# Kernel tuning notes

Measured on AMD Instinct MI355X. Metric: run time of the kernel, lower is better.

## Reference

```python
import jax, jax.numpy as jnp
import numpy as np

B, N = 128, 512            # graphs per batch, nodes (seq len) per graph
NODE_VOCAB, APP_VOCAB = 30000, 5000
D, R, K = 128, 512, 3      # embed_size, rec_embed dim, Chebyshev order
EPS = 1e-12


def setup_inputs() -> dict:
    key = jax.random.key(0)
    ks = jax.random.split(key, 8)
    return {
        # all tokens nonzero -> every position is a valid node (item > 0 filter passes)
        "input_seq": jax.random.randint(ks[0], (B, N), 1, NODE_VOCAB),
        "recd_token": jax.random.randint(ks[1], (B, N), 1, APP_VOCAB),
        "embed_table": jax.random.normal(ks[2], (NODE_VOCAB, D), jnp.float32) * 0.02,
        "rec_embed_table": jax.random.normal(ks[3], (APP_VOCAB, R), jnp.float32) * 0.02,
        "cheb_w1": jax.random.normal(ks[4], (K, D, D), jnp.float32) / np.sqrt(D),
        "cheb_b1": jnp.zeros((D,), jnp.float32),
        "cheb_w2": jax.random.normal(ks[5], (K, D, D), jnp.float32) / np.sqrt(D),
        "cheb_b2": jnp.zeros((D,), jnp.float32),
    }


def _prop_matrix(app_emb):
    """Per-sample scaled Laplacian L_hat = -D^{-1/2} A D^{-1/2}.

    app_emb: [B,N,R] (detached upstream, matching recd.detach() in the source).
    Adjacency: cosine-sim matrix, entries below the mean of the nonzero strict
    upper triangle zeroed. ChebConv receives edge_index only -> binary weights,
    self-loops removed, default lambda_max=2 -> L_hat = -A_norm.
    """
    app_feat = app_emb / jnp.maximum(
        jnp.linalg.norm(app_emb, axis=-1, keepdims=True), EPS)      # F.normalize dim=1
    A = jnp.einsum('bnr,bmr->bnm', app_feat, app_feat)              # [B,N,N]
    upper = jnp.triu(A, 1)
    cnt = jnp.sum(upper != 0, axis=(1, 2)).astype(A.dtype)
    mean = jnp.sum(upper, axis=(1, 2)) / jnp.maximum(cnt, 1.0)      # [B]
    A = jnp.where(A < mean[:, None, None], 0.0, A)
    adj = (A != 0).astype(A.dtype) * (1.0 - jnp.eye(N, dtype=A.dtype))  # binary, no self-loops
    deg = adj.sum(-1)                                               # [B,N]
    dinv = jnp.where(deg > 0, jax.lax.rsqrt(jnp.maximum(deg, EPS)), 0.0)
    return -(dinv[:, :, None] * adj * dinv[:, None, :])             # [B,N,N]


def _cheb(x, S, w, b):
    # Chebyshev recurrence T0=x, T1=Sx, T2=2S T1 - T0
    tx0 = x
    tx1 = jnp.einsum('bnm,bmd->bnd', S, tx0)
    tx2 = 2.0 * jnp.einsum('bnm,bmd->bnd', S, tx1) - tx0
    return (jnp.einsum('bnd,de->bne', tx0, w[0])
            + jnp.einsum('bnd,de->bne', tx1, w[1])
            + jnp.einsum('bnd,de->bne', tx2, w[2]) + b)


def reference(input_seq, recd_token, embed_table, rec_embed_table,
              cheb_w1, cheb_b1, cheb_w2, cheb_b2):
    app_emb = rec_embed_table[recd_token]                           # [B,N,R]
    # adjacency built from detached embeddings (recd.detach() in source)
    S = jax.lax.stop_gradient(_prop_matrix(jax.lax.stop_gradient(app_emb)))
    x = embed_table[input_seq]                                      # [B,N,D]
    x = jax.nn.relu(_cheb(x, S, cheb_w1, cheb_b1))
    x = jax.nn.relu(_cheb(x, S, cheb_w2, cheb_b2))
    out = jnp.concatenate([x, app_emb], axis=-1)                    # [B,N,D+R]
    return out.reshape(B * N, D + R)                                # Batch'ed node features
```

## Files before the change

### kernel.cpp

```cpp
#include <hip/hip_runtime.h>
#include <hip/hip_bf16.h>

typedef __attribute__((ext_vector_type(8))) unsigned short ushort8;
typedef __attribute__((ext_vector_type(4))) unsigned short bf16x4;
typedef __attribute__((ext_vector_type(8))) short short8;
typedef __attribute__((ext_vector_type(4))) float f32x4;
typedef __attribute__((ext_vector_type(2))) unsigned long long u64x2;

#define DEV __device__ __forceinline__

DEV unsigned short f2bf(float f) {
    unsigned u = __builtin_bit_cast(unsigned, f);
    return (unsigned short)((u + 0x7fffu + ((u >> 16) & 1u)) >> 16);
}
DEV float bf2f(unsigned short h) {
    unsigned u = ((unsigned)h) << 16;
    return __builtin_bit_cast(float, u);
}
DEV float wred(float v) {
#pragma unroll
    for (int m = 32; m > 0; m >>= 1) v += __shfl_xor(v, m, 64);
    return v;
}

constexpr int N_ = 512, D_ = 128, R_ = 512;
constexpr long NN2 = (long)N_ * N_;

DEV void gll16(const void* g, void* l) {
    __builtin_amdgcn_global_load_lds(
        (const __attribute__((address_space(1))) unsigned*)g,
        (__attribute__((address_space(3))) unsigned*)l, 16, 0, 0);
}


__global__ __launch_bounds__(256) void k_front(const int* __restrict__ recd,
                                               const float* __restrict__ rtab,
                                               const int* __restrict__ seq,
                                               const float* __restrict__ etab,
                                               const float* __restrict__ w1,
                                               const float* __restrict__ w2,
                                               float* __restrict__ out,
                                               unsigned short* __restrict__ feat,
                                               unsigned short* __restrict__ x,
                                               unsigned short* __restrict__ wT) {
    int bid = blockIdx.x, tid = threadIdx.x;
    if (bid < 16384) {
        int lane = tid & 63, w = tid >> 6;
        long r = (long)bid * 4 + w;
        int tok = recd[r];
        const float* src = rtab + (long)tok * R_;
        int j = lane * 8;
        float4 v0 = *(const float4*)(src + j);
        float4 v1 = *(const float4*)(src + j + 4);
        float ssq = v0.x*v0.x + v0.y*v0.y + v0.z*v0.z + v0.w*v0.w
                  + v1.x*v1.x + v1.y*v1.y + v1.z*v1.z + v1.w*v1.w;
        ssq = wred(ssq);
        float sc = 1.0f / fmaxf(sqrtf(ssq), 1e-12f);
        float* o = out + r * 640 + 128 + j;
        *(float4*)o = v0;
        *(float4*)(o + 4) = v1;
        ushort8 u;
        u[0]=f2bf(v0.x*sc); u[1]=f2bf(v0.y*sc); u[2]=f2bf(v0.z*sc); u[3]=f2bf(v0.w*sc);
        u[4]=f2bf(v1.x*sc); u[5]=f2bf(v1.y*sc); u[6]=f2bf(v1.z*sc); u[7]=f2bf(v1.w*sc);
        *(ushort8*)(feat + r * R_ + j) = u;
    } else if (bid < 20480) {
        long e8 = ((long)(bid - 16384) * 256 + tid) * 8;
        long r = e8 >> 7;
        int d0 = (int)(e8 & 127);
        int tok = seq[r];
        const float* src = etab + (long)tok * D_ + d0;
        float4 v0 = *(const float4*)src, v1 = *(const float4*)(src + 4);
        ushort8 u;
        u[0]=f2bf(v0.x); u[1]=f2bf(v0.y); u[2]=f2bf(v0.z); u[3]=f2bf(v0.w);
        u[4]=f2bf(v1.x); u[5]=f2bf(v1.y); u[6]=f2bf(v1.z); u[7]=f2bf(v1.w);
        *(ushort8*)(x + e8) = u;
    } else {
        int o = (bid - 20480) * 256 + tid;
        int l = o / 49152;
        int rr = o - l * 49152;
        int mat = rr >> 14;
        int e2 = rr & 16383;
        int e = e2 >> 7, d = e2 & 127;
        const float* w = l ? w2 : w1;
        float v;
        if (mat == 0)      v = w[d * 128 + e] - w[32768 + d * 128 + e];
        else if (mat == 1) v = w[16384 + d * 128 + e];
        else               v = 2.0f * w[32768 + d * 128 + e];
        wT[o] = f2bf(v);
    }
}


DEV void stage_rowmajor(const unsigned short* base, long ld, int k0,
                        unsigned short* dst, int tid) {
#pragma unroll
    for (int i = 0; i < 4; ++i) {
        int u = i * 256 + tid;
        int r = u >> 3, c = (u & 7) * 8;
        gll16(base + (long)r * ld + k0 + c,
              dst + i * 2048 + (tid & 448) * 8);
    }
}

DEV void gemm_bt_core(const unsigned short* Abase, long ldA,
                      const unsigned short* Bbase, long ldB, int K,
                      unsigned short* As, unsigned short* Bs,
                      f32x4 acc[4][4], bool dual) {
    int tid = threadIdx.x, lane = tid & 63, wave = tid >> 6;
    int wm = wave >> 1, wn = wave & 1;
    int fr = lane & 15, ko = (lane >> 4) * 8;
    const unsigned short* Bsrc = dual ? Bs : As;
    for (int k0 = 0; k0 < K; k0 += 64) {
        __syncthreads();
        stage_rowmajor(Abase, ldA, k0, As, tid);
        if (dual) stage_rowmajor(Bbase, ldB, k0, Bs, tid);
        __syncthreads();
#pragma unroll
        for (int ks = 0; ks < 2; ++ks) {
            short8 a[4], b[4];
#pragma unroll
            for (int m = 0; m < 4; ++m)
                a[m] = *(const short8*)(As + (wm * 64 + m * 16 + fr) * 64 + ks * 32 + ko);
#pragma unroll
            for (int n = 0; n < 4; ++n)
                b[n] = *(const short8*)(Bsrc + (wn * 64 + n * 16 + fr) * 64 + ks * 32 + ko);
#pragma unroll
            for (int m = 0; m < 4; ++m)
#pragma unroll
                for (int n = 0; n < 4; ++n)
                    acc[m][n] = __builtin_amdgcn_mfma_f32_16x16x32_bf16(
                        a[m], b[n], acc[m][n], 0, 0, 0);
        }
    }
}


__global__ __launch_bounds__(256) void k_adj(const unsigned short* __restrict__ feat,
                                             unsigned short* __restrict__ Abf,
                                             float* __restrict__ psum,
                                             float* __restrict__ pcnt) {
    __shared__ unsigned short As[128 * 64], Bs[128 * 64];
    __shared__ float sred[4], cred[4];
    int g = blockIdx.x;
    int r = g & 7, q = g >> 3;
    int q10 = q / 10;
    int b = r + (q10 << 3);
    int t = q - q10 * 10;
    int tm = (t < 4) ? 0 : (t < 7) ? 1 : (t < 9) ? 2 : 3;
    int tn = t - (tm * (9 - tm)) / 2 + tm;
    bool diag = (tm == tn);
    const unsigned short* fb = feat + (long)b * NN2;
    f32x4 acc[4][4] = {};
    gemm_bt_core(fb + (long)tm * 128 * R_, R_, fb + (long)tn * 128 * R_, R_, R_,
                 As, Bs, acc, !diag);
    int tid = threadIdx.x, lane = tid & 63, wave = tid >> 6;
    int wm = wave >> 1, wn = wave & 1;
    float s = 0.f, c = 0.f;
    unsigned short* Ab = Abf + (long)b * NN2;
#pragma unroll
    for (int m = 0; m < 4; ++m)
#pragma unroll
        for (int n = 0; n < 4; ++n) {
            f32x4 v = acc[m][n];
            int gj = tn * 128 + wn * 64 + n * 16 + (lane & 15);
            int gi0 = tm * 128 + wm * 64 + m * 16 + (lane >> 4) * 4;
            bf16x4 tw;
#pragma unroll
            for (int qq = 0; qq < 4; ++qq) {
                int gi = gi0 + qq;
                unsigned short bv = f2bf(v[qq]);
                Ab[(long)gi * N_ + gj] = bv;
                tw[qq] = bv;
                if (gj > gi) {
                    s += v[qq];
                    c += (v[qq] != 0.0f) ? 1.0f : 0.0f;
                }
            }
            if (!diag)
                *(bf16x4*)(Ab + (long)gj * N_ + gi0) = tw;
        }
    s = wred(s);
    c = wred(c);
    if (lane == 0) { sred[wave] = s; cred[wave] = c; }
    __syncthreads();
    if (tid == 0) {
        psum[b * 16 + t] = sred[0] + sred[1] + sred[2] + sred[3];
        pcnt[b * 16 + t] = cred[0] + cred[1] + cred[2] + cred[3];
    }
}

__global__ __launch_bounds__(256) void k_degtrs(unsigned short* __restrict__ Abf,
                                                const float* __restrict__ psum,
                                                const float* __restrict__ pcnt,
                                                const unsigned short* __restrict__ xin,
                                                float* __restrict__ dinv,
                                                unsigned short* __restrict__ pT) {
    __shared__ unsigned char mb[4][64];
    __shared__ float sdinv[64];
    __shared__ unsigned short t[64 * 128];
    int bid = blockIdx.x;
    int b = bid >> 3, tn = bid & 7;
    int tid = threadIdx.x, lane = tid & 63, w = tid >> 6;
    float s = 0.f, c = 0.f;
#pragma unroll
    for (int k = 0; k < 10; ++k) { s += psum[b * 16 + k]; c += pcnt[b * 16 + k]; }
    float m = s / fmaxf(c, 1.0f);
#pragma unroll 1
    for (int i = 0; i < 16; ++i) {
        int rl = w * 16 + i;
        long r = (long)b * 512 + tn * 64 + rl;
        int ig = tn * 64 + rl;
        ushort8 v = *(const ushort8*)(Abf + r * 512 + lane * 8);
        unsigned byt = 0;
        int cnt = 0;
#pragma unroll
        for (int k = 0; k < 8; ++k) {
            float f = bf2f(v[k]);
            int j = lane * 8 + k;
            bool keep = (f >= m) && (f != 0.0f) && (j != ig);
            byt |= (keep ? 1u : 0u) << k;
            cnt += keep ? 1 : 0;
        }
        mb[w][lane] = (unsigned char)byt;
        float fc = wred((float)cnt);
        if (lane < 8) {
            unsigned long long mword = *(const unsigned long long*)&mb[w][lane * 8];
            *(unsigned long long*)((unsigned char*)Abf + r * 1024 + lane * 8) = mword;
        }
        if (lane == 8) {
            float dv = (fc > 0.f) ? rsqrtf(fc) : 0.f;
            dinv[r] = dv;
            sdinv[rl] = dv;
        }
    }
    __syncthreads();
    const unsigned short* ib = xin + ((long)b * 512 + tn * 64) * 128;
    unsigned short* ob = pT + (long)b * 65536 + tn * 64;
#pragma unroll
    for (int i = 0; i < 4; ++i) {
        int u = i * 256 + tid;
        int n = u >> 4, g = u & 15;
        float sc = sdinv[n];
        ushort8 v = *(const ushort8*)(ib + n * 128 + g * 8);
        ushort8 sv;
#pragma unroll
        for (int tt = 0; tt < 8; ++tt) sv[tt] = f2bf(bf2f(v[tt]) * sc);
        int gs = g ^ ((n >> 3) & 7);
        *(ushort8*)(t + n * 128 + gs * 8) = sv;
    }
    __syncthreads();
#pragma unroll
    for (int i = 0; i < 4; ++i) {
        int u = i * 256 + tid;
        int d = u >> 3, n8 = (u & 7) * 8;
        ushort8 v;
#pragma unroll
        for (int tt = 0; tt < 8; ++tt) {
            int n = n8 + tt;
            int g = (d >> 3) ^ ((n >> 3) & 7);
            v[tt] = t[n * 128 + g * 8 + (d & 7)];
        }
        *(ushort8*)(ob + (long)d * 512 + n8) = v;
    }
}

__global__ __launch_bounds__(256) void k_sxm(const unsigned short* __restrict__ Abf,
                                             const float* __restrict__ dinv,
                                             const unsigned short* __restrict__ pT,
                                             unsigned short* __restrict__ outN,
                                             unsigned short* __restrict__ outT) {
    __shared__ __align__(16) unsigned short Bs[128 * 64];
    __shared__ __align__(8) unsigned short lut4[16 * 4];
    int tid = threadIdx.x, lane = tid & 63, wave = tid >> 6;
    if (tid < 16) {
        unsigned long long e = 0;
#pragma unroll
        for (int j = 0; j < 4; ++j)
            if ((tid >> j) & 1) e |= 0x3F80ull << (16 * j);
        *(unsigned long long*)(lut4 + tid * 4) = e;
    }
    int g = blockIdx.x;
    int r = g & 7, q = g >> 3;
    int b = r + ((q >> 2) << 3);
    int tm = q & 3;
    int wm = wave >> 1, wn = wave & 1;
    int fr = lane & 15, ko = (lane >> 4) * 8;
    const unsigned char* mbase = (const unsigned char*)Abf + (long)b * 524288;
    const unsigned short* pb = pT + (long)b * 65536;
    f32x4 acc[4][4] = {};
    for (int k0 = 0; k0 < 512; k0 += 64) {
        __syncthreads();
        stage_rowmajor(pb, 512, k0, Bs, tid);
        unsigned long long mw[4];
#pragma unroll
        for (int m = 0; m < 4; ++m) {
            int row = tm * 128 + wm * 64 + m * 16 + fr;
            mw[m] = *(const unsigned long long*)(mbase + (long)row * 1024 + (k0 >> 3));
        }
        __syncthreads();
#pragma unroll
        for (int ks = 0; ks < 2; ++ks) {
            short8 a4[4], b4[4];
#pragma unroll
            for (int m = 0; m < 4; ++m) {
                unsigned w32 = (unsigned)(mw[m] >> (ks * 32));
                unsigned byt = (w32 >> ko) & 255u;
                unsigned long long lo = *(const unsigned long long*)(lut4 + (byt & 15u) * 4);
                unsigned long long hi = *(const unsigned long long*)(lut4 + (byt >> 4) * 4);
                u64x2 tt; tt[0] = lo; tt[1] = hi;
                a4[m] = __builtin_bit_cast(short8, tt);
            }
#pragma unroll
            for (int n = 0; n < 4; ++n)
                b4[n] = *(const short8*)(Bs + (wn * 64 + n * 16 + fr) * 64 + ks * 32 + ko);
#pragma unroll
            for (int m = 0; m < 4; ++m)
#pragma unroll
                for (int n = 0; n < 4; ++n)
                    acc[m][n] = __builtin_amdgcn_mfma_f32_16x16x32_bf16(
                        a4[m], b4[n], acc[m][n], 0, 0, 0);
        }
    }
    unsigned short* on = outN + (long)b * 65536;
#pragma unroll
    for (int m = 0; m < 4; ++m) {
        int gi0 = tm * 128 + wm * 64 + m * 16 + ((lane >> 4) << 2);
        float4 dv = *(const float4*)(dinv + (long)b * 512 + gi0);
#pragma unroll
        for (int n = 0; n < 4; ++n) {
            int gj = wn * 64 + n * 16 + fr;
            bf16x4 tw;
#pragma unroll
            for (int qq = 0; qq < 4; ++qq) {
                float dq = (&dv.x)[qq];
                float t1v = -dq * acc[m][n][qq];
                on[(long)(gi0 + qq) * 128 + gj] = f2bf(t1v);
                tw[qq] = f2bf(dq * t1v);
            }
            *(bf16x4*)(outT + (long)b * 65536 + (long)gj * 512 + gi0) = tw;
        }
    }
}

template <int LAYER>
__global__ __launch_bounds__(256) void k_sxp(const unsigned short* __restrict__ Abf,
                                             const float* __restrict__ dinv,
                                             const unsigned short* __restrict__ pTin,
                                             const unsigned short* __restrict__ t0,
                                             const unsigned short* __restrict__ t1,
                                             const unsigned short* __restrict__ wTl,
                                             const float* __restrict__ bias,
                                             unsigned short* __restrict__ ybf,
                                             unsigned short* __restrict__ pTout,
                                             float* __restrict__ out) {
    __shared__ __align__(16) unsigned short As[128 * 64], Bs[128 * 64];
    __shared__ __align__(16) unsigned short uLds[128 * 132];
    __shared__ __align__(8) unsigned short lut4[16 * 4];
    int tid = threadIdx.x, lane = tid & 63, wave = tid >> 6;
    if (tid < 16) {
        unsigned long long e = 0;
#pragma unroll
        for (int j = 0; j < 4; ++j)
            if ((tid >> j) & 1) e |= 0x3F80ull << (16 * j);
        *(unsigned long long*)(lut4 + tid * 4) = e;
    }
    int g = blockIdx.x;
    int r = g & 7, q = g >> 3;
    int b = r + ((q >> 2) << 3);
    int tm = q & 3;
    int wm = wave >> 1, wn = wave & 1;
    int fr = lane & 15, ko = (lane >> 4) * 8;
    {
        const unsigned char* mbase = (const unsigned char*)Abf + (long)b * 524288;
        const unsigned short* pb = pTin + (long)b * 65536;
        f32x4 acc[4][4] = {};
        for (int k0 = 0; k0 < 512; k0 += 64) {
            __syncthreads();
            stage_rowmajor(pb, 512, k0, Bs, tid);
            unsigned long long mw[4];
#pragma unroll
            for (int m = 0; m < 4; ++m) {
                int row = tm * 128 + wm * 64 + m * 16 + fr;
                mw[m] = *(const unsigned long long*)(mbase + (long)row * 1024 + (k0 >> 3));
            }
            __syncthreads();
#pragma unroll
            for (int ks = 0; ks < 2; ++ks) {
                short8 a4[4], b4[4];
#pragma unroll
                for (int m = 0; m < 4; ++m) {
                    unsigned w32 = (unsigned)(mw[m] >> (ks * 32));
                    unsigned byt = (w32 >> ko) & 255u;
                    unsigned long long lo = *(const unsigned long long*)(lut4 + (byt & 15u) * 4);
                    unsigned long long hi = *(const unsigned long long*)(lut4 + (byt >> 4) * 4);
                    u64x2 tt; tt[0] = lo; tt[1] = hi;
                    a4[m] = __builtin_bit_cast(short8, tt);
                }
#pragma unroll
                for (int n = 0; n < 4; ++n)
                    b4[n] = *(const short8*)(Bs + (wn * 64 + n * 16 + fr) * 64 + ks * 32 + ko);
#pragma unroll
                for (int m = 0; m < 4; ++m)
#pragma unroll
                    for (int n = 0; n < 4; ++n)
                        acc[m][n] = __builtin_amdgcn_mfma_f32_16x16x32_bf16(
                            a4[m], b4[n], acc[m][n], 0, 0, 0);
            }
        }
#pragma unroll
        for (int m = 0; m < 4; ++m) {
            int li0 = wm * 64 + m * 16 + ((lane >> 4) << 2);
            float4 dv = *(const float4*)(dinv + (long)b * 512 + tm * 128 + li0);
#pragma unroll
            for (int n = 0; n < 4; ++n) {
                int gj = wn * 64 + n * 16 + fr;
#pragma unroll
                for (int qq = 0; qq < 4; ++qq)
                    uLds[(li0 + qq) * 132 + gj] = f2bf(-(&dv.x)[qq] * acc[m][n][qq]);
            }
        }
    }
    long row0 = (long)b * 512 + tm * 128;
    f32x4 acc2[4][4] = {};
    gemm_bt_core(t0 + row0 * D_, D_, wTl,          D_, D_, As, Bs, acc2, true);
    gemm_bt_core(t1 + row0 * D_, D_, wTl + 16384,  D_, D_, As, Bs, acc2, true);
    for (int s2 = 0; s2 < 2; ++s2) {
        __syncthreads();
        stage_rowmajor(wTl + 32768, 128, s2 * 64, Bs, tid);
        __syncthreads();
#pragma unroll
        for (int ks = 0; ks < 2; ++ks) {
            short8 a[4], bfr[4];
#pragma unroll
            for (int m = 0; m < 4; ++m)
                a[m] = *(const short8*)(uLds + (wm * 64 + m * 16 + fr) * 132 + s2 * 64 + ks * 32 + ko);
#pragma unroll
            for (int n = 0; n < 4; ++n)
                bfr[n] = *(const short8*)(Bs + (wn * 64 + n * 16 + fr) * 64 + ks * 32 + ko);
#pragma unroll
            for (int m = 0; m < 4; ++m)
#pragma unroll
                for (int n = 0; n < 4; ++n)
                    acc2[m][n] = __builtin_amdgcn_mfma_f32_16x16x32_bf16(
                        a[m], bfr[n], acc2[m][n], 0, 0, 0);
        }
    }
#pragma unroll
    for (int m = 0; m < 4; ++m) {
        long gr0 = row0 + wm * 64 + m * 16 + ((lane >> 4) << 2);
        float4 dv;
        if (LAYER == 1) dv = *(const float4*)(dinv + gr0);
#pragma unroll
        for (int n = 0; n < 4; ++n) {
            int gj = wn * 64 + n * 16 + (lane & 15);
            bf16x4 tw;
#pragma unroll
            for (int qq = 0; qq < 4; ++qq) {
                long gr = gr0 + qq;
                float v = fmaxf(acc2[m][n][qq] + bias[gj], 0.0f);
                if (LAYER == 1) {
                    ybf[gr * D_ + gj] = f2bf(v);
                    tw[qq] = f2bf((&dv.x)[qq] * v);
                } else {
                    out[gr * 640 + gj] = v;
                }
            }
            if (LAYER == 1)
                *(bf16x4*)(pTout + (gr0 >> 9) * 65536 + (long)gj * 512 + (gr0 & 511)) = tw;
        }
    }
}


extern "C" void kernel_launch(void* const* d_in, const int* in_sizes, int n_in,
                              void* d_out, int out_size, void* d_ws, size_t ws_size,
                              hipStream_t stream) {
    const int* seq    = (const int*)d_in[0];
    const int* recd   = (const int*)d_in[1];
    const float* etab = (const float*)d_in[2];
    const float* rtab = (const float*)d_in[3];
    const float* w1   = (const float*)d_in[4];
    const float* b1   = (const float*)d_in[5];
    const float* w2   = (const float*)d_in[6];
    const float* b2   = (const float*)d_in[7];
    float* out = (float*)d_out;
    char* ws = (char*)d_ws;

    if (ws_size < 151470592u) return;

    unsigned short* Abf  = (unsigned short*)(ws);
    unsigned short* feat = (unsigned short*)(ws + 67108864);
    unsigned short* pTa  = (unsigned short*)(ws + 67108864);
    unsigned short* pTb  = (unsigned short*)(ws + 83886080);
    unsigned short* t1   = (unsigned short*)(ws + 100663296);
    unsigned short* xbf  = (unsigned short*)(ws + 134217728);
    unsigned short* wT   = (unsigned short*)(ws + 150994944);
    float* psum = (float*)(ws + 151191552);
    float* pcnt = (float*)(ws + 151199744);
    float* dinv = (float*)(ws + 151208448);

    k_front<<<20864, 256, 0, stream>>>(recd, rtab, seq, etab, w1, w2, out, feat, xbf, wT);
    k_adj<<<1280, 256, 0, stream>>>(feat, Abf, psum, pcnt);
    k_degtrs<<<1024, 256, 0, stream>>>(Abf, psum, pcnt, xbf, dinv, pTa);
    k_sxm<<<512, 256, 0, stream>>>(Abf, dinv, pTa, t1, pTb);
    k_sxp<1><<<512, 256, 0, stream>>>(Abf, dinv, pTb, xbf, t1, wT, b1,
                                      xbf, pTa, nullptr);
    k_sxm<<<512, 256, 0, stream>>>(Abf, dinv, pTa, t1, pTb);
    k_sxp<2><<<512, 256, 0, stream>>>(Abf, dinv, pTb, xbf, t1, wT + 49152, b2,
                                      nullptr, nullptr, out);
}
```

Measured before the change: 233.2 us.

## Gather bf16 rec-embedding table directly in adjacency GEMM; widen k-step to 128

Instead of writing a normalized bf16 feature tensor for every node (B*N*R), the front kernel converts the small rec-embedding table to bf16 once and stores per-node inverse norms. The adjacency GEMM gathers rows from the bf16 table by token directly into LDS and applies the norm scaling in the epilogue, removing a large intermediate write and read. The S·X kernels also stage 128-wide K panels per iteration, halving the barrier count at the cost of more LDS. Risks include uncoalesced gather loads and rounding differences, since normalization is now applied after the bf16 dot product.

```diff
diff --git a/kernel.cpp b/kernel.cpp
--- a/kernel.cpp
+++ b/kernel.cpp
@@ -40,9 +40,10 @@
                                                const float* __restrict__ w1,
                                                const float* __restrict__ w2,
                                                float* __restrict__ out,
-                                               unsigned short* __restrict__ feat,
                                                unsigned short* __restrict__ x,
-                                               unsigned short* __restrict__ wT) {
+                                               unsigned short* __restrict__ wT,
+                                               unsigned short* __restrict__ rtb,
+                                               float* __restrict__ rnorm) {
     int bid = blockIdx.x, tid = threadIdx.x;
     if (bid < 16384) {
         int lane = tid & 63, w = tid >> 6;
@@ -55,14 +56,10 @@
         float ssq = v0.x*v0.x + v0.y*v0.y + v0.z*v0.z + v0.w*v0.w
                   + v1.x*v1.x + v1.y*v1.y + v1.z*v1.z + v1.w*v1.w;
         ssq = wred(ssq);
-        float sc = 1.0f / fmaxf(sqrtf(ssq), 1e-12f);
         float* o = out + r * 640 + 128 + j;
         *(float4*)o = v0;
         *(float4*)(o + 4) = v1;
-        ushort8 u;
-        u[0]=f2bf(v0.x*sc); u[1]=f2bf(v0.y*sc); u[2]=f2bf(v0.z*sc); u[3]=f2bf(v0.w*sc);
-        u[4]=f2bf(v1.x*sc); u[5]=f2bf(v1.y*sc); u[6]=f2bf(v1.z*sc); u[7]=f2bf(v1.w*sc);
-        *(ushort8*)(feat + r * R_ + j) = u;
+        if (lane == 0) rnorm[r] = 1.0f / fmaxf(sqrtf(ssq), 1e-12f);
     } else if (bid < 20480) {
         long e8 = ((long)(bid - 16384) * 256 + tid) * 8;
         long r = e8 >> 7;
@@ -74,7 +71,7 @@
         u[0]=f2bf(v0.x); u[1]=f2bf(v0.y); u[2]=f2bf(v0.z); u[3]=f2bf(v0.w);
         u[4]=f2bf(v1.x); u[5]=f2bf(v1.y); u[6]=f2bf(v1.z); u[7]=f2bf(v1.w);
         *(ushort8*)(x + e8) = u;
-    } else {
+    } else if (bid < 20864) {
         int o = (bid - 20480) * 256 + tid;
         int l = o / 49152;
         int rr = o - l * 49152;
@@ -87,6 +84,13 @@
         else if (mat == 1) v = w[16384 + d * 128 + e];
         else               v = 2.0f * w[32768 + d * 128 + e];
         wT[o] = f2bf(v);
+    } else {
+        long e8 = ((long)(bid - 20864) * 256 + tid) * 8;
+        float4 v0 = *(const float4*)(rtab + e8), v1 = *(const float4*)(rtab + e8 + 4);
+        ushort8 u;
+        u[0]=f2bf(v0.x); u[1]=f2bf(v0.y); u[2]=f2bf(v0.z); u[3]=f2bf(v0.w);
+        u[4]=f2bf(v1.x); u[5]=f2bf(v1.y); u[6]=f2bf(v1.z); u[7]=f2bf(v1.w);
+        *(ushort8*)(rtb + e8) = u;
     }
 }
 
@@ -98,6 +102,28 @@
         int u = i * 256 + tid;
         int r = u >> 3, c = (u & 7) * 8;
         gll16(base + (long)r * ld + k0 + c,
+              dst + i * 2048 + (tid & 448) * 8);
+    }
+}
+
+DEV void stage_panel128(const unsigned short* base, int k0,
+                        unsigned short* dst, int tid) {
+#pragma unroll
+    for (int i = 0; i < 8; ++i) {
+        int u = i * 256 + tid;
+        int r = u >> 4, c = (u & 15) * 8;
+        gll16(base + (long)r * 512 + k0 + c,
+              dst + i * 2048 + (tid & 448) * 8);
+    }
+}
+
+DEV void stage_gather(const unsigned short* tab, const int* toks, int k0,
+                      unsigned short* dst, int tid) {
+#pragma unroll
+    for (int i = 0; i < 4; ++i) {
+        int u = i * 256 + tid;
+        int r = u >> 3, c = (u & 7) * 8;
+        gll16(tab + (long)toks[r] * 512 + k0 + c,
               dst + i * 2048 + (tid & 448) * 8);
     }
 }
@@ -135,50 +161,81 @@
 }
 
 
-__global__ __launch_bounds__(256) void k_adj(const unsigned short* __restrict__ feat,
+__global__ __launch_bounds__(256) void k_adj(const unsigned short* __restrict__ rtb,
+                                             const int* __restrict__ recd,
+                                             const float* __restrict__ rnorm,
                                              unsigned short* __restrict__ Abf,
                                              float* __restrict__ psum,
                                              float* __restrict__ pcnt) {
-    __shared__ unsigned short As[128 * 64], Bs[128 * 64];
+    __shared__ __align__(16) unsigned short As[128 * 64], Bs[128 * 64];
+    __shared__ int toks[256];
     __shared__ float sred[4], cred[4];
     int g = blockIdx.x;
-    int r = g & 7, q = g >> 3;
+    int r8 = g & 7, q = g >> 3;
     int q10 = q / 10;
-    int b = r + (q10 << 3);
+    int b = r8 + (q10 << 3);
     int t = q - q10 * 10;
     int tm = (t < 4) ? 0 : (t < 7) ? 1 : (t < 9) ? 2 : 3;
     int tn = t - (tm * (9 - tm)) / 2 + tm;
     bool diag = (tm == tn);
-    const unsigned short* fb = feat + (long)b * NN2;
+    int tid = threadIdx.x, lane = tid & 63, wave = tid >> 6;
+    if (tid < 128) toks[tid] = recd[b * 512 + tm * 128 + tid];
+    else           toks[tid] = recd[b * 512 + tn * 128 + (tid - 128)];
+    int wm = wave >> 1, wn = wave & 1;
+    int fr = lane & 15, ko = (lane >> 4) * 8;
     f32x4 acc[4][4] = {};
-    gemm_bt_core(fb + (long)tm * 128 * R_, R_, fb + (long)tn * 128 * R_, R_, R_,
-                 As, Bs, acc, !diag);
-    int tid = threadIdx.x, lane = tid & 63, wave = tid >> 6;
-    int wm = wave >> 1, wn = wave & 1;
+    for (int k0 = 0; k0 < 512; k0 += 64) {
+        __syncthreads();
+        stage_gather(rtb, toks, k0, As, tid);
+        if (!diag) stage_gather(rtb, toks + 128, k0, Bs, tid);
+        __syncthreads();
+        const unsigned short* Bsrc = diag ? As : Bs;
+#pragma unroll
+        for (int ks = 0; ks < 2; ++ks) {
+            short8 a[4], bb[4];
+#pragma unroll
+            for (int m = 0; m < 4; ++m)
+                a[m] = *(const short8*)(As + (wm * 64 + m * 16 + fr) * 64 + ks * 32 + ko);
+#pragma unroll
+            for (int n = 0; n < 4; ++n)
+                bb[n] = *(const short8*)(Bsrc + (wn * 64 + n * 16 + fr) * 64 + ks * 32 + ko);
+#pragma unroll
+            for (int m = 0; m < 4; ++m)
+#pragma unroll
+                for (int n = 0; n < 4; ++n)
+                    acc[m][n] = __builtin_amdgcn_mfma_f32_16x16x32_bf16(
+                        a[m], bb[n], acc[m][n], 0, 0, 0);
+        }
+    }
     float s = 0.f, c = 0.f;
     unsigned short* Ab = Abf + (long)b * NN2;
-#pragma unroll
-    for (int m = 0; m < 4; ++m)
+    const float* rnb = rnorm + (long)b * 512;
+#pragma unroll
+    for (int m = 0; m < 4; ++m) {
+        int gi0 = tm * 128 + wm * 64 + m * 16 + (lane >> 4) * 4;
+        float4 rni = *(const float4*)(rnb + gi0);
 #pragma unroll
         for (int n = 0; n < 4; ++n) {
+            int gj = tn * 128 + wn * 64 + n * 16 + fr;
+            float rj = rnb[gj];
             f32x4 v = acc[m][n];
-            int gj = tn * 128 + wn * 64 + n * 16 + (lane & 15);
-            int gi0 = tm * 128 + wm * 64 + m * 16 + (lane >> 4) * 4;
             bf16x4 tw;
 #pragma unroll
             for (int qq = 0; qq < 4; ++qq) {
                 int gi = gi0 + qq;
-                unsigned short bv = f2bf(v[qq]);
+                float vv = v[qq] * (&rni.x)[qq] * rj;
+                unsigned short bv = f2bf(vv);
                 Ab[(long)gi * N_ + gj] = bv;
                 tw[qq] = bv;
                 if (gj > gi) {
-                    s += v[qq];
-                    c += (v[qq] != 0.0f) ? 1.0f : 0.0f;
+                    s += vv;
+                    c += (vv != 0.0f) ? 1.0f : 0.0f;
                 }
             }
             if (!diag)
                 *(bf16x4*)(Ab + (long)gj * N_ + gi0) = tw;
         }
+    }
     s = wred(s);
     c = wred(c);
     if (lane == 0) { sred[wave] = s; cred[wave] = c; }
@@ -269,7 +326,7 @@
                                              const unsigned short* __restrict__ pT,
                                              unsigned short* __restrict__ outN,
                                              unsigned short* __restrict__ outT) {
-    __shared__ __align__(16) unsigned short Bs[128 * 64];
+    __shared__ __align__(16) unsigned short Bs[128 * 128];
     __shared__ __align__(8) unsigned short lut4[16 * 4];
     int tid = threadIdx.x, lane = tid & 63, wave = tid >> 6;
     if (tid < 16) {
@@ -288,22 +345,22 @@
     const unsigned char* mbase = (const unsigned char*)Abf + (long)b * 524288;
     const unsigned short* pb = pT + (long)b * 65536;
     f32x4 acc[4][4] = {};
-    for (int k0 = 0; k0 < 512; k0 += 64) {
-        __syncthreads();
-        stage_rowmajor(pb, 512, k0, Bs, tid);
-        unsigned long long mw[4];
+    for (int k0 = 0; k0 < 512; k0 += 128) {
+        __syncthreads();
+        stage_panel128(pb, k0, Bs, tid);
+        u64x2 mw[4];
 #pragma unroll
         for (int m = 0; m < 4; ++m) {
             int row = tm * 128 + wm * 64 + m * 16 + fr;
-            mw[m] = *(const unsigned long long*)(mbase + (long)row * 1024 + (k0 >> 3));
-        }
-        __syncthreads();
-#pragma unroll
-        for (int ks = 0; ks < 2; ++ks) {
+            mw[m] = *(const u64x2*)(mbase + (long)row * 1024 + (k0 >> 3));
+        }
+        __syncthreads();
+#pragma unroll
+        for (int ks = 0; ks < 4; ++ks) {
             short8 a4[4], b4[4];
 #pragma unroll
             for (int m = 0; m < 4; ++m) {
-                unsigned w32 = (unsigned)(mw[m] >> (ks * 32));
+                unsigned w32 = (unsigned)(mw[m][ks >> 1] >> ((ks & 1) * 32));
                 unsigned byt = (w32 >> ko) & 255u;
                 unsigned long long lo = *(const unsigned long long*)(lut4 + (byt & 15u) * 4);
                 unsigned long long hi = *(const unsigned long long*)(lut4 + (byt >> 4) * 4);
@@ -312,7 +369,7 @@
             }
 #pragma unroll
             for (int n = 0; n < 4; ++n)
-                b4[n] = *(const short8*)(Bs + (wn * 64 + n * 16 + fr) * 64 + ks * 32 + ko);
+                b4[n] = *(const short8*)(Bs + (wn * 64 + n * 16 + fr) * 128 + ks * 32 + ko);
 #pragma unroll
             for (int m = 0; m < 4; ++m)
 #pragma unroll
@@ -353,7 +410,7 @@
                                              unsigned short* __restrict__ ybf,
                                              unsigned short* __restrict__ pTout,
                                              float* __restrict__ out) {
-    __shared__ __align__(16) unsigned short As[128 * 64], Bs[128 * 64];
+    __shared__ __align__(16) unsigned short AsBs[128 * 128];
     __shared__ __align__(16) unsigned short uLds[128 * 132];
     __shared__ __align__(8) unsigned short lut4[16 * 4];
     int tid = threadIdx.x, lane = tid & 63, wave = tid >> 6;
@@ -374,22 +431,22 @@
         const unsigned char* mbase = (const unsigned char*)Abf + (long)b * 524288;
         const unsigned short* pb = pTin + (long)b * 65536;
         f32x4 acc[4][4] = {};
-        for (int k0 = 0; k0 < 512; k0 += 64) {
+        for (int k0 = 0; k0 < 512; k0 += 128) {
             __syncthreads();
-            stage_rowmajor(pb, 512, k0, Bs, tid);
-            unsigned long long mw[4];
+            stage_panel128(pb, k0, AsBs, tid);
+            u64x2 mw[4];
 #pragma unroll
             for (int m = 0; m < 4; ++m) {
                 int row = tm * 128 + wm * 64 + m * 16 + fr;
-                mw[m] = *(const unsigned long long*)(mbase + (long)row * 1024 + (k0 >> 3));
+                mw[m] = *(const u64x2*)(mbase + (long)row * 1024 + (k0 >> 3));
             }
             __syncthreads();
 #pragma unroll
-            for (int ks = 0; ks < 2; ++ks) {
+            for (int ks = 0; ks < 4; ++ks) {
                 short8 a4[4], b4[4];
 #pragma unroll
                 for (int m = 0; m < 4; ++m) {
-                    unsigned w32 = (unsigned)(mw[m] >> (ks * 32));
+                    unsigned w32 = (unsigned)(mw[m][ks >> 1] >> ((ks & 1) * 32));
                     unsigned byt = (w32 >> ko) & 255u;
                     unsigned long long lo = *(const unsigned long long*)(lut4 + (byt & 15u) * 4);
                     unsigned long long hi = *(const unsigned long long*)(lut4 + (byt >> 4) * 4);
@@ -398,7 +455,7 @@
                 }
 #pragma unroll
                 for (int n = 0; n < 4; ++n)
-                    b4[n] = *(const short8*)(Bs + (wn * 64 + n * 16 + fr) * 64 + ks * 32 + ko);
+                    b4[n] = *(const short8*)(AsBs + (wn * 64 + n * 16 + fr) * 128 + ks * 32 + ko);
 #pragma unroll
                 for (int m = 0; m < 4; ++m)
 #pragma unroll
@@ -420,6 +477,8 @@
             }
         }
     }
+    unsigned short* As = AsBs;
+    unsigned short* Bs = AsBs + 8192;
     long row0 = (long)b * 512 + tm * 128;
     f32x4 acc2[4][4] = {};
     gemm_bt_core(t0 + row0 * D_, D_, wTl,          D_, D_, As, Bs, acc2, true);
@@ -489,18 +548,20 @@
     if (ws_size < 151470592u) return;
 
     unsigned short* Abf  = (unsigned short*)(ws);
-    unsigned short* feat = (unsigned short*)(ws + 67108864);
     unsigned short* pTa  = (unsigned short*)(ws + 67108864);
     unsigned short* pTb  = (unsigned short*)(ws + 83886080);
     unsigned short* t1   = (unsigned short*)(ws + 100663296);
+    unsigned short* rtb  = (unsigned short*)(ws + 117440512);
+    float* rnorm         = (float*)(ws + 122683392);
     unsigned short* xbf  = (unsigned short*)(ws + 134217728);
     unsigned short* wT   = (unsigned short*)(ws + 150994944);
     float* psum = (float*)(ws + 151191552);
     float* pcnt = (float*)(ws + 151199744);
     float* dinv = (float*)(ws + 151208448);
 
-    k_front<<<20864, 256, 0, stream>>>(recd, rtab, seq, etab, w1, w2, out, feat, xbf, wT);
-    k_adj<<<1280, 256, 0, stream>>>(feat, Abf, psum, pcnt);
+    k_front<<<22114, 256, 0, stream>>>(recd, rtab, seq, etab, w1, w2,
+                                       out, xbf, wT, rtb, rnorm);
+    k_adj<<<1280, 256, 0, stream>>>(rtb, recd, rnorm, Abf, psum, pcnt);
     k_degtrs<<<1024, 256, 0, stream>>>(Abf, psum, pcnt, xbf, dinv, pTa);
     k_sxm<<<512, 256, 0, stream>>>(Abf, dinv, pTa, t1, pTb);
     k_sxp<1><<<512, 256, 0, stream>>>(Abf, dinv, pTb, xbf, t1, wT, b1,
```

Result: faster. 225.9 us (-3.1%).
